# Optimization experiments

Hardware: AMD Instinct MI355X
Metric: run time of the kernel (lower is better)

## Reference

```python
import jax, jax.numpy as jnp
import numpy as np

D_MODEL = 2048
NUM_HEADS = 16
D_FF = 8192
EPS = 1e-5


def setup_inputs() -> dict:
    key = jax.random.key(0)
    ks = jax.random.split(key, 9)
    s = 0.02
    return {
        "x": jax.random.normal(ks[0], (2, 2048, D_MODEL), dtype=jnp.float32),
        "wq": jax.random.normal(ks[1], (D_MODEL, D_MODEL), dtype=jnp.float32) * s,
        "wk": jax.random.normal(ks[2], (D_MODEL, D_MODEL), dtype=jnp.float32) * s,
        "wv": jax.random.normal(ks[3], (D_MODEL, D_MODEL), dtype=jnp.float32) * s,
        "wo": jax.random.normal(ks[4], (D_MODEL, D_MODEL), dtype=jnp.float32) * s,
        "w1": jax.random.normal(ks[5], (D_FF, D_MODEL), dtype=jnp.float32) * s,
        "w2": jax.random.normal(ks[6], (D_MODEL, D_FF), dtype=jnp.float32) * s,
        "g1": jnp.ones((D_MODEL,), dtype=jnp.float32),
        "g2": jnp.ones((D_MODEL,), dtype=jnp.float32),
    }


def rmsnorm(a, g):
    rms = jnp.sqrt(jnp.sum(a * a, axis=-1, keepdims=True) / a.shape[-1] + EPS)
    return a / rms * g


def attention(xn, wq, wk, wv, wo):
    B, S, D = xn.shape
    H, dk = NUM_HEADS, D // NUM_HEADS
    # Linear weights are (out, in); y = x @ W^T
    q = (xn @ wq.T).reshape(B, S, H, dk).transpose(0, 2, 1, 3)  # bhsd
    k = (xn @ wk.T).reshape(B, S, H, dk).transpose(0, 2, 1, 3)
    v = (xn @ wv.T).reshape(B, S, H, dk).transpose(0, 2, 1, 3)
    scores = jnp.einsum("bhqd,bhkd->bhqk", q, k) * (dk ** -0.5)
    causal = jnp.triu(jnp.ones((S, S), dtype=bool), k=1)
    scores = jnp.where(causal, -jnp.inf, scores)
    probs = jax.nn.softmax(scores, axis=-1)
    out = jnp.einsum("bhqk,bhkd->bhqd", probs, v)
    out = out.transpose(0, 2, 1, 3).reshape(B, S, D)
    return out @ wo.T


def reference(x, wq, wk, wv, wo, w1, w2, g1, g2):
    x = x + attention(rmsnorm(x, g1), wq, wk, wv, wo)
    h = jax.nn.gelu(rmsnorm(x, g2) @ w1.T, approximate=False)
    x = x + h @ w2.T
    return x
```

## Files before the change

kernel.cpp:

```cpp
#include <hip/hip_runtime.h>
#include <hip/hip_bf16.h>
#include <math.h>

#define D_MODEL 2048
#define SEQ     2048
#define BATCH   2
#define NHEAD   16
#define DK      128
#define DFF     8192
#define MROWS   (BATCH*SEQ)

typedef short short8 __attribute__((ext_vector_type(8)));
typedef float f32x4  __attribute__((ext_vector_type(4)));

__device__ __forceinline__ short f2bf(float f) {
  union { __hip_bfloat16 b; short s; } u;
  u.b = __float2bfloat16(f);
  return u.s;
}

#define MF(a, b, c) __builtin_amdgcn_mfma_f32_16x16x32_bf16(a, b, c, 0, 0, 0)
#define BAR()   asm volatile("s_barrier" ::: "memory")
#define LGKM0() { asm volatile("s_waitcnt lgkmcnt(0)" ::: "memory"); __builtin_amdgcn_sched_barrier(0); }
#define STG(gptr, ldsbyte) { \
    unsigned _m0v = (unsigned)__builtin_amdgcn_readfirstlane((int)(ldsbyte)); \
    asm volatile("s_mov_b32 m0, %1\n\tglobal_load_lds_dwordx4 %0, off" \
                 :: "v"(gptr), "s"(_m0v) : "memory"); }

__global__ __launch_bounds__(256) void rmsnorm_k(const float* __restrict__ x,
                                                 const float* __restrict__ g,
                                                 short* __restrict__ o) {
  const int row = blockIdx.x;
  const int t = threadIdx.x;
  const float4* xr = (const float4*)(x + (size_t)row * D_MODEL);
  const float4* gr = (const float4*)g;
  float4 v0 = xr[2*t], v1 = xr[2*t+1];
  float s = v0.x*v0.x + v0.y*v0.y + v0.z*v0.z + v0.w*v0.w
          + v1.x*v1.x + v1.y*v1.y + v1.z*v1.z + v1.w*v1.w;
  #pragma unroll
  for (int off = 1; off < 64; off <<= 1) s += __shfl_xor(s, off);
  __shared__ float red[4];
  if ((t & 63) == 0) red[t >> 6] = s;
  __syncthreads();
  float tot = red[0] + red[1] + red[2] + red[3];
  float inv = rsqrtf(tot * (1.0f / D_MODEL) + 1e-5f);
  float4 g0 = gr[2*t], g1v = gr[2*t+1];
  short8 ov;
  ov[0] = f2bf(v0.x * inv * g0.x);
  ov[1] = f2bf(v0.y * inv * g0.y);
  ov[2] = f2bf(v0.z * inv * g0.z);
  ov[3] = f2bf(v0.w * inv * g0.w);
  ov[4] = f2bf(v1.x * inv * g1v.x);
  ov[5] = f2bf(v1.y * inv * g1v.y);
  ov[6] = f2bf(v1.z * inv * g1v.z);
  ov[7] = f2bf(v1.w * inv * g1v.w);
  *((short8*)(o + (size_t)row * D_MODEL) + t) = ov;
}

__global__ __launch_bounds__(256) void f2b_k(const float* __restrict__ src,
                                             short* __restrict__ dst, int n8) {
  int i = blockIdx.x * 256 + threadIdx.x;
  if (i >= n8) return;
  const float4* s4 = (const float4*)src + 2 * (size_t)i;
  float4 a = s4[0], b = s4[1];
  short8 o = { f2bf(a.x), f2bf(a.y), f2bf(a.z), f2bf(a.w),
               f2bf(b.x), f2bf(b.y), f2bf(b.z), f2bf(b.w) };
  *((short8*)dst + i) = o;
}

__global__ __launch_bounds__(256) void combine_k(const float* p0, const float* p1,
                                                 const float* r, float* o, int n4) {
  int i = blockIdx.x * 256 + threadIdx.x;
  if (i >= n4) return;
  const float4 a = ((const float4*)p0)[i];
  const float4 b = ((const float4*)p1)[i];
  const float4 c = ((const float4*)r)[i];
  float4 d;
  d.x = a.x + b.x + c.x; d.y = a.y + b.y + c.y;
  d.z = a.z + b.z + c.z; d.w = a.w + b.w + c.w;
  ((float4*)o)[i] = d;
}

template<int EPI, int SPLIT>
__global__ __launch_bounds__(512, 2) void gemm256(const short* __restrict__ A,
                                                  const short* __restrict__ Bp,
                                                  void* Cv,
                                                  const float* __restrict__ resid,
                                                  int M, int N, int K,
                                                  int lda, int ldb, int nbx) {
  __shared__ __align__(16) short As[2][2][128 * 64];
  __shared__ __align__(16) short Bs[2][2][128 * 64];
  const int nk = K >> 6;
  const int cpx = gridDim.x >> 3;
  const int lin = (blockIdx.x & 7) * cpx + (blockIdx.x >> 3);
  const int bx = lin % nbx;
  int row2 = lin / nbx, by, ks = 0;
  if (SPLIT) { ks = row2 & 1; by = row2 >> 1; } else { by = row2; }
  const int m0 = bx * 256, n0 = by * 256;
  if (SPLIT) { A += (size_t)ks * K; Bp += (size_t)ks * K; }

  const int t = threadIdx.x, w = t >> 6, lane = t & 63, lr = lane & 15, lg = lane >> 4;
  const int wm = w >> 2, wn = w & 3;
  const unsigned aByte = (unsigned)(size_t)(const __attribute__((address_space(3))) short*)&As[0][0][0];
  const unsigned bByte = (unsigned)(size_t)(const __attribute__((address_space(3))) short*)&Bs[0][0][0];
  const unsigned wOff = (unsigned)(w * 1024);

  const int r = t >> 3, c8 = t & 7;
  const int sw = (c8 ^ (r & 7)) << 3;
  const short* pA0 = A  + (size_t)(m0 + r)       * lda + sw;
  const short* pA1 = A  + (size_t)(m0 + 128 + r) * lda + sw;
  const short* pB0 = Bp + (size_t)(n0 + r)       * ldb + sw;
  const short* pB1 = Bp + (size_t)(n0 + 128 + r) * ldb + sw;
  const size_t l64A = (size_t)64 * lda, l64B = (size_t)64 * ldb;

  f32x4 acc[8][4];
  const f32x4 z4 = {0.f, 0.f, 0.f, 0.f};
  #pragma unroll
  for (int m = 0; m < 8; ++m)
    #pragma unroll
    for (int n = 0; n < 4; ++n) acc[m][n] = z4;

  STG(pA0,        aByte + wOff);                 STG(pA0 + l64A,      aByte + 8192 + wOff);
  STG(pA1,        aByte + 16384 + wOff);         STG(pA1 + l64A,      aByte + 16384 + 8192 + wOff);
  STG(pB0,        bByte + wOff);                 STG(pB0 + l64B,      bByte + 8192 + wOff);
  STG(pB1,        bByte + 16384 + wOff);         STG(pB1 + l64B,      bByte + 16384 + 8192 + wOff);
  if (nk > 1) {
    STG(pB0 + 64, bByte + 32768 + wOff);         STG(pB0 + 64 + l64B, bByte + 32768 + 8192 + wOff);
    STG(pB1 + 64, bByte + 32768 + 16384 + wOff); STG(pB1 + 64 + l64B, bByte + 32768 + 16384 + 8192 + wOff);
    STG(pA0 + 64, aByte + 32768 + wOff);         STG(pA0 + 64 + l64A, aByte + 32768 + 8192 + wOff);
    asm volatile("s_waitcnt vmcnt(6)" ::: "memory");
  } else {
    asm volatile("s_waitcnt vmcnt(0)" ::: "memory");
  }
  BAR();

  for (int T = 0; T < nk; ++T) {
    const int p = T & 1, q = p ^ 1;
    const unsigned aS = aByte + (unsigned)p * 32768u, aQ = aByte + (unsigned)q * 32768u;
    const unsigned bS = bByte + (unsigned)p * 32768u;

    if (T + 1 < nk) {
      const short* s = pA1 + (size_t)(T + 1) * 64;
      STG(s, aQ + 16384u + wOff); STG(s + l64A, aQ + 16384u + 8192u + wOff);
    }
    short8 bk0[4], bk1[4], aA[4];
    #pragma unroll
    for (int n = 0; n < 4; ++n) {
      int br = wn * 64 + n * 16 + lr;
      const short* bp = &Bs[p][br >> 7][(br & 127) * 64];
      bk0[n] = *(const short8*)&bp[(lg * 8)      ^ ((br & 7) << 3)];
      bk1[n] = *(const short8*)&bp[(32 + lg * 8) ^ ((br & 7) << 3)];
    }
    #pragma unroll
    for (int m = 0; m < 4; ++m) {
      int ar = m * 16 + lr;
      aA[m] = *(const short8*)&As[p][wm][ar * 64 + ((lg * 8) ^ ((ar & 7) << 3))];
    }
    BAR(); LGKM0();
    __builtin_amdgcn_s_setprio(1);
    #pragma unroll
    for (int m = 0; m < 4; ++m)
      #pragma unroll
      for (int n = 0; n < 4; ++n) acc[m][n] = MF(aA[m], bk0[n], acc[m][n]);
    __builtin_amdgcn_s_setprio(0);
    BAR();

    if (T + 2 < nk) {
      const short* s = pB0 + (size_t)(T + 2) * 64;
      STG(s, bS + wOff); STG(s + l64B, bS + 8192u + wOff);
    }
    short8 aB[4], aC[4];
    #pragma unroll
    for (int m = 0; m < 4; ++m) {
      int ar = 64 + m * 16 + lr;
      aB[m] = *(const short8*)&As[p][wm][ar * 64 + ((lg * 8) ^ ((ar & 7) << 3))];
      int ar2 = m * 16 + lr;
      aC[m] = *(const short8*)&As[p][wm][ar2 * 64 + ((32 + lg * 8) ^ ((ar2 & 7) << 3))];
    }
    BAR(); LGKM0();
    __builtin_amdgcn_s_setprio(1);
    #pragma unroll
    for (int m = 0; m < 4; ++m)
      #pragma unroll
      for (int n = 0; n < 4; ++n) acc[m + 4][n] = MF(aB[m], bk0[n], acc[m + 4][n]);
    __builtin_amdgcn_s_setprio(0);
    BAR();

    if (T + 2 < nk) {
      const short* s = pB1 + (size_t)(T + 2) * 64;
      STG(s, bS + 16384u + wOff); STG(s + l64B, bS + 16384u + 8192u + wOff);
    }
    short8 aD[4];
    #pragma unroll
    for (int m = 0; m < 4; ++m) {
      int ar = 64 + m * 16 + lr;
      aD[m] = *(const short8*)&As[p][wm][ar * 64 + ((32 + lg * 8) ^ ((ar & 7) << 3))];
    }
    BAR(); LGKM0();
    __builtin_amdgcn_s_setprio(1);
    #pragma unroll
    for (int m = 0; m < 4; ++m)
      #pragma unroll
      for (int n = 0; n < 4; ++n) acc[m][n] = MF(aC[m], bk1[n], acc[m][n]);
    __builtin_amdgcn_s_setprio(0);
    BAR();

    if (T + 2 < nk) {
      const short* s = pA0 + (size_t)(T + 2) * 64;
      STG(s, aS + wOff); STG(s + l64A, aS + 8192u + wOff);
    }
    BAR(); LGKM0();
    __builtin_amdgcn_s_setprio(1);
    #pragma unroll
    for (int m = 0; m < 4; ++m)
      #pragma unroll
      for (int n = 0; n < 4; ++n) acc[m + 4][n] = MF(aD[m], bk1[n], acc[m + 4][n]);
    __builtin_amdgcn_s_setprio(0);

    if (T + 2 < nk)      { asm volatile("s_waitcnt vmcnt(6)" ::: "memory"); BAR(); }
    else if (T + 1 < nk) { asm volatile("s_waitcnt vmcnt(0)" ::: "memory"); BAR(); }
  }

  float* Cf = (float*)Cv;
  if (SPLIT) Cf += (size_t)ks * ((size_t)M * N);
  #pragma unroll
  for (int m = 0; m < 8; ++m)
    #pragma unroll
    for (int n = 0; n < 4; ++n)
      #pragma unroll
      for (int rr = 0; rr < 4; ++rr) {
        int row = m0 + wm * 128 + m * 16 + lg * 4 + rr;
        int col = n0 + wn * 64 + n * 16 + lr;
        size_t idx = (size_t)row * N + col;
        float vv = acc[m][n][rr];
        if (EPI == 0) {
          ((short*)Cv)[idx] = f2bf(vv);
        } else if (EPI == 1) {
          float gl = 0.5f * vv * (1.0f + erff(vv * 0.70710678118654752f));
          ((short*)Cv)[idx] = f2bf(gl);
        } else if (EPI == 2) {
          ((float*)Cv)[idx] = vv + resid[idx];
        } else {
          Cf[idx] = vv;
        }
      }
}

__global__ __launch_bounds__(256) void vtrans(const short* __restrict__ QKV,
                                              short* __restrict__ VT) {
  const int st = blockIdx.x;
  const int bh = blockIdx.y;
  const int b = bh >> 4, h = bh & 15;
  const int t = threadIdx.x;
  __shared__ __align__(16) short T[64 * 128];
  const short* Vsrc = QKV + ((size_t)b * SEQ) * 6144 + 2 * D_MODEL + h * DK;
  {
    int r = t >> 4, c = (t & 15) * 8;
    #pragma unroll
    for (int i = 0; i < 4; ++i) {
      int rr = r + 16 * i;
      uint4 vv = *(const uint4*)(Vsrc + (size_t)(st * 64 + rr) * 6144 + c);
      *(uint4*)&T[rr * 128 + (c ^ (((rr >> 3) & 7) << 3))] = vv;
    }
  }
  __syncthreads();
  short* dst = VT + ((size_t)bh * DK) * SEQ + st * 64;
  {
    int c2 = (t & 7) * 8;
    #pragma unroll
    for (int i = 0; i < 4; ++i) {
      int d = (t >> 3) + 32 * i;
      short8 ov;
      #pragma unroll
      for (int j = 0; j < 8; ++j)
        ov[j] = T[(c2 + j) * 128 + (d ^ ((((c2 + j) >> 3) & 7) << 3))];
      *(short8*)(dst + (size_t)d * SEQ + c2) = ov;
    }
  }
}

__global__ __launch_bounds__(512, 2) void attn3(const short* __restrict__ QKV,
                                                const short* __restrict__ VT,
                                                short* __restrict__ O) {
  const float SC = 0.12751743f;
  const int a = blockIdx.x, bh = blockIdx.y;
  const int b = bh >> 4, h = bh & 15;
  const int t = threadIdx.x, w = t >> 6, lane = t & 63, lr = lane & 15, lg = lane >> 4;
  const short* Qp = QKV + ((size_t)b * SEQ) * 6144 + h * DK;
  const short* Kp = Qp + D_MODEL;
  const short* Vp = VT + ((size_t)bh * DK) * SEQ;
  __shared__ __align__(16) short Ks[2][64 * 128];
  __shared__ __align__(16) short Vs[2][128 * 64];
  __shared__ __align__(16) short Ps[8][16][72];

  const int krr = t >> 4, kcc = (t & 15) * 8;
  const int vdd = t >> 3, vcc = (t & 7) * 8;
  const f32x4 z4 = {0.f, 0.f, 0.f, 0.f};

  for (int sub = 0; sub < 2; ++sub) {
    const int ts = sub ? (15 - a) : a;
    const int nt = 2 * ts + 2;
    const int qrow0 = ts * 128 + w * 16;

    short8 qf[4];
    #pragma unroll
    for (int ki = 0; ki < 4; ++ki)
      qf[ki] = *(const short8*)(Qp + (size_t)(qrow0 + lr) * 6144 + ki * 32 + lg * 8);

    f32x4 acc[8];
    #pragma unroll
    for (int nd = 0; nd < 8; ++nd) acc[nd] = z4;
    float mrow[4], lsum[4];
    #pragma unroll
    for (int r = 0; r < 4; ++r) { mrow[r] = -INFINITY; lsum[r] = 0.f; }

    uint4 krg[2], vrg[2];
    #pragma unroll
    for (int i = 0; i < 2; ++i) {
      krg[i] = *(const uint4*)(Kp + (size_t)(krr + 32 * i) * 6144 + kcc);
      vrg[i] = *(const uint4*)(Vp + (size_t)(vdd + 64 * i) * SEQ + vcc);
    }
    __syncthreads();
    #pragma unroll
    for (int i = 0; i < 2; ++i) {
      int r = krr + 32 * i;
      *(uint4*)&Ks[0][(r * 128 + kcc) ^ ((r & 7) << 3)] = krg[i];
      int d = vdd + 64 * i;
      *(uint4*)&Vs[0][(d * 64 + vcc) ^ ((d & 7) << 3)] = vrg[i];
    }
    __syncthreads();

    int cur = 0;
    for (int tt = 0; tt < nt; ++tt) {
      const bool pre = (tt + 1 < nt);
      if (pre) {
        #pragma unroll
        for (int i = 0; i < 2; ++i) {
          krg[i] = *(const uint4*)(Kp + (size_t)((tt + 1) * 64 + krr + 32 * i) * 6144 + kcc);
          vrg[i] = *(const uint4*)(Vp + (size_t)(vdd + 64 * i) * SEQ + (tt + 1) * 64 + vcc);
        }
      }

      f32x4 sf[4] = {z4, z4, z4, z4};
      #pragma unroll
      for (int ki = 0; ki < 4; ++ki) {
        #pragma unroll
        for (int nk = 0; nk < 4; ++nk) {
          int rr = nk * 16 + lr;
          short8 kf = *(const short8*)&Ks[cur][(rr * 128 + ki * 32 + lg * 8) ^ ((rr & 7) << 3)];
          sf[nk] = MF(qf[ki], kf, sf[nk]);
        }
      }

      const bool diag = (tt * 64 + 63 > qrow0);
      #pragma unroll
      for (int r = 0; r < 4; ++r) {
        int qg = qrow0 + lg * 4 + r;
        float s0 = sf[0][r] * SC, s1 = sf[1][r] * SC, s2 = sf[2][r] * SC, s3 = sf[3][r] * SC;
        if (diag) {
          int c0 = tt * 64 + lr;
          s0 = (c0      <= qg) ? s0 : -3.0e38f;
          s1 = (c0 + 16 <= qg) ? s1 : -3.0e38f;
          s2 = (c0 + 32 <= qg) ? s2 : -3.0e38f;
          s3 = (c0 + 48 <= qg) ? s3 : -3.0e38f;
        }
        float mx = fmaxf(fmaxf(s0, s1), fmaxf(s2, s3));
        mx = fmaxf(mx, __shfl_xor(mx, 1));
        mx = fmaxf(mx, __shfl_xor(mx, 2));
        mx = fmaxf(mx, __shfl_xor(mx, 4));
        mx = fmaxf(mx, __shfl_xor(mx, 8));
        float mnew = fmaxf(mrow[r], mx);
        float alpha = exp2f(mrow[r] - mnew);
        mrow[r] = mnew;
        float p0 = exp2f(s0 - mnew), p1 = exp2f(s1 - mnew),
              p2 = exp2f(s2 - mnew), p3 = exp2f(s3 - mnew);
        lsum[r] = lsum[r] * alpha + ((p0 + p1) + (p2 + p3));
        #pragma unroll
        for (int nd = 0; nd < 8; ++nd) acc[nd][r] *= alpha;
        short* pr = &Ps[w][lg * 4 + r][0];
        pr[lr]      = f2bf(p0);
        pr[16 + lr] = f2bf(p1);
        pr[32 + lr] = f2bf(p2);
        pr[48 + lr] = f2bf(p3);
      }
      asm volatile("s_waitcnt lgkmcnt(0)" ::: "memory");
      __builtin_amdgcn_sched_barrier(0);

      short8 pf0 = *(const short8*)&Ps[w][lr][lg * 8];
      short8 pf1 = *(const short8*)&Ps[w][lr][32 + lg * 8];
      #pragma unroll
      for (int nd = 0; nd < 8; ++nd) {
        int rr = nd * 16 + lr;
        short8 vf0 = *(const short8*)&Vs[cur][(rr * 64 + lg * 8) ^ ((rr & 7) << 3)];
        short8 vf1 = *(const short8*)&Vs[cur][(rr * 64 + 32 + lg * 8) ^ ((rr & 7) << 3)];
        acc[nd] = MF(pf0, vf0, acc[nd]);
        acc[nd] = MF(pf1, vf1, acc[nd]);
      }
      __syncthreads();
      if (pre) {
        #pragma unroll
        for (int i = 0; i < 2; ++i) {
          int r = krr + 32 * i;
          *(uint4*)&Ks[cur ^ 1][(r * 128 + kcc) ^ ((r & 7) << 3)] = krg[i];
          int d = vdd + 64 * i;
          *(uint4*)&Vs[cur ^ 1][(d * 64 + vcc) ^ ((d & 7) << 3)] = vrg[i];
        }
      }
      __syncthreads();
      cur ^= 1;
    }

    float inv[4];
    #pragma unroll
    for (int r = 0; r < 4; ++r) {
      float ls = lsum[r];
      ls += __shfl_xor(ls, 1);
      ls += __shfl_xor(ls, 2);
      ls += __shfl_xor(ls, 4);
      ls += __shfl_xor(ls, 8);
      inv[r] = 1.0f / ls;
    }
    #pragma unroll
    for (int nd = 0; nd < 8; ++nd)
      #pragma unroll
      for (int r = 0; r < 4; ++r) {
        int row = qrow0 + lg * 4 + r;
        O[(size_t)(b * SEQ + row) * D_MODEL + h * DK + nd * 16 + lr] = f2bf(acc[nd][r] * inv[r]);
      }
  }
}

template<int EPI>
__global__ __launch_bounds__(256) void gemm_bt(const short* __restrict__ A,
                                               const float* __restrict__ B,
                                               void* Cv,
                                               const float* resid,
                                               int M, int N, int K) {
  __shared__ __align__(16) short As[128][72];
  __shared__ __align__(16) short Bs[128][72];
  const int t = threadIdx.x;
  const int m0 = blockIdx.x * 128, n0 = blockIdx.y * 128;
  const int wave = t >> 6, lane = t & 63, lr = lane & 15, lg = lane >> 4;
  const int wr = (wave >> 1) * 64, wc = (wave & 1) * 64;

  f32x4 acc[4][4];
  const f32x4 z4 = {0.f, 0.f, 0.f, 0.f};
  #pragma unroll
  for (int m = 0; m < 4; ++m)
    #pragma unroll
    for (int n = 0; n < 4; ++n) acc[m][n] = z4;

  int ar[4], ac[4];
  #pragma unroll
  for (int i = 0; i < 4; ++i) { int u = t + 256*i; ar[i] = u >> 3; ac[i] = (u & 7) * 8; }

  for (int k0 = 0; k0 < K; k0 += 64) {
    #pragma unroll
    for (int i = 0; i < 4; ++i) {
      uint4 va = *(const uint4*)(A + (size_t)(m0 + ar[i]) * K + k0 + ac[i]);
      *(uint4*)&As[ar[i]][ac[i]] = va;
    }
    #pragma unroll
    for (int i = 0; i < 4; ++i) {
      const float4* bp = (const float4*)(B + (size_t)(n0 + ar[i]) * K + k0 + ac[i]);
      float4 b0 = bp[0], b1 = bp[1];
      short8 pb = { f2bf(b0.x), f2bf(b0.y), f2bf(b0.z), f2bf(b0.w),
                    f2bf(b1.x), f2bf(b1.y), f2bf(b1.z), f2bf(b1.w) };
      *(short8*)&Bs[ar[i]][ac[i]] = pb;
    }
    __syncthreads();
    #pragma unroll
    for (int kk = 0; kk < 64; kk += 32) {
      short8 af[4], bfr[4];
      #pragma unroll
      for (int m = 0; m < 4; ++m) af[m]  = *(const short8*)&As[wr + m*16 + lr][kk + lg*8];
      #pragma unroll
      for (int n = 0; n < 4; ++n) bfr[n] = *(const short8*)&Bs[wc + n*16 + lr][kk + lg*8];
      #pragma unroll
      for (int m = 0; m < 4; ++m)
        #pragma unroll
        for (int n = 0; n < 4; ++n)
          acc[m][n] = MF(af[m], bfr[n], acc[m][n]);
    }
    __syncthreads();
  }

  #pragma unroll
  for (int m = 0; m < 4; ++m)
    #pragma unroll
    for (int n = 0; n < 4; ++n)
      #pragma unroll
      for (int r = 0; r < 4; ++r) {
        int row = m0 + wr + m*16 + lg*4 + r;
        int col = n0 + wc + n*16 + lr;
        size_t idx = (size_t)row * N + col;
        float vv = acc[m][n][r];
        if (EPI == 0) {
          ((short*)Cv)[idx] = f2bf(vv);
        } else if (EPI == 1) {
          float gl = 0.5f * vv * (1.0f + erff(vv * 0.70710678118654752f));
          ((short*)Cv)[idx] = f2bf(gl);
        } else {
          ((float*)Cv)[idx] = vv + resid[idx];
        }
      }
}

__global__ __launch_bounds__(256) void attn_k(const short* __restrict__ Q,
                                              const short* __restrict__ K,
                                              const short* __restrict__ V,
                                              short* __restrict__ O) {
  const float scale = 0.08838834764831845f;
  const int qt = blockIdx.x;
  const int bh = blockIdx.y;
  const int b = bh >> 4, h = bh & 15;
  const size_t base = ((size_t)b * SEQ) * D_MODEL + (size_t)h * DK;
  const int t = threadIdx.x, wave = t >> 6, lane = t & 63, lr = lane & 15, lg = lane >> 4;

  __shared__ __align__(16) short Ks[32][136];
  __shared__ __align__(16) short Vt[128][40];
  __shared__ __align__(16) short Ps[4][32][40];

  const int qrow0 = qt * 128 + wave * 32;
  short8 qf[2][4];
  #pragma unroll
  for (int mq = 0; mq < 2; ++mq)
    #pragma unroll
    for (int ki = 0; ki < 4; ++ki)
      qf[mq][ki] = *(const short8*)(Q + base + (size_t)(qrow0 + mq*16 + lr) * D_MODEL + ki*32 + lg*8);

  f32x4 acc[2][8];
  const f32x4 z4 = {0.f, 0.f, 0.f, 0.f};
  #pragma unroll
  for (int mq = 0; mq < 2; ++mq)
    #pragma unroll
    for (int nd = 0; nd < 8; ++nd) acc[mq][nd] = z4;
  float mrow[2][4], lsum[2][4];
  #pragma unroll
  for (int mq = 0; mq < 2; ++mq)
    #pragma unroll
    for (int r = 0; r < 4; ++r) { mrow[mq][r] = -INFINITY; lsum[mq][r] = 0.f; }

  const int lastt = qt * 4 + 3;
  for (int tt = 0; tt <= lastt; ++tt) {
    #pragma unroll
    for (int i = 0; i < 2; ++i) {
      int u = t + 256*i; int r = u >> 4; int c = (u & 15) * 8;
      *(uint4*)&Ks[r][c] = *(const uint4*)(K + base + (size_t)(tt*32 + r) * D_MODEL + c);
      uint4 vv = *(const uint4*)(V + base + (size_t)(tt*32 + r) * D_MODEL + c);
      const short* sv = (const short*)&vv;
      #pragma unroll
      for (int j = 0; j < 8; ++j) Vt[c + j][r] = sv[j];
    }
    __syncthreads();
    if (tt <= qt * 4 + wave) {
      f32x4 sf[2][2] = {{z4, z4}, {z4, z4}};
      #pragma unroll
      for (int ki = 0; ki < 4; ++ki) {
        short8 kf0 = *(const short8*)&Ks[lr][ki*32 + lg*8];
        short8 kf1 = *(const short8*)&Ks[16 + lr][ki*32 + lg*8];
        sf[0][0] = MF(qf[0][ki], kf0, sf[0][0]);
        sf[0][1] = MF(qf[0][ki], kf1, sf[0][1]);
        sf[1][0] = MF(qf[1][ki], kf0, sf[1][0]);
        sf[1][1] = MF(qf[1][ki], kf1, sf[1][1]);
      }
      #pragma unroll
      for (int mq = 0; mq < 2; ++mq) {
        #pragma unroll
        for (int r = 0; r < 4; ++r) {
          int qg = qrow0 + mq*16 + lg*4 + r;
          float s0 = sf[mq][0][r] * scale;
          float s1 = sf[mq][1][r] * scale;
          if (tt*32 + lr > qg)       s0 = -INFINITY;
          if (tt*32 + 16 + lr > qg)  s1 = -INFINITY;
          float mx = fmaxf(s0, s1);
          mx = fmaxf(mx, __shfl_xor(mx, 1));
          mx = fmaxf(mx, __shfl_xor(mx, 2));
          mx = fmaxf(mx, __shfl_xor(mx, 4));
          mx = fmaxf(mx, __shfl_xor(mx, 8));
          float mnew = fmaxf(mrow[mq][r], mx);
          float alpha = __expf(mrow[mq][r] - mnew);
          mrow[mq][r] = mnew;
          float p0 = __expf(s0 - mnew);
          float p1 = __expf(s1 - mnew);
          float ps = p0 + p1;
          ps += __shfl_xor(ps, 1);
          ps += __shfl_xor(ps, 2);
          ps += __shfl_xor(ps, 4);
          ps += __shfl_xor(ps, 8);
          lsum[mq][r] = lsum[mq][r] * alpha + ps;
          #pragma unroll
          for (int nd = 0; nd < 8; ++nd) acc[mq][nd][r] *= alpha;
          Ps[wave][mq*16 + lg*4 + r][lr]      = f2bf(p0);
          Ps[wave][mq*16 + lg*4 + r][16 + lr] = f2bf(p1);
        }
      }
      asm volatile("s_waitcnt lgkmcnt(0)" ::: "memory");
      short8 pf0 = *(const short8*)&Ps[wave][lr][lg*8];
      short8 pf1 = *(const short8*)&Ps[wave][16 + lr][lg*8];
      #pragma unroll
      for (int nd = 0; nd < 8; ++nd) {
        short8 vf = *(const short8*)&Vt[nd*16 + lr][lg*8];
        acc[0][nd] = MF(pf0, vf, acc[0][nd]);
        acc[1][nd] = MF(pf1, vf, acc[1][nd]);
      }
    }
    __syncthreads();
  }

  #pragma unroll
  for (int mq = 0; mq < 2; ++mq)
    #pragma unroll
    for (int nd = 0; nd < 8; ++nd)
      #pragma unroll
      for (int r = 0; r < 4; ++r) {
        int row = qrow0 + mq*16 + lg*4 + r;
        O[base + (size_t)row * D_MODEL + nd*16 + lr] = f2bf(acc[mq][nd][r] / lsum[mq][r]);
      }
}

extern "C" void kernel_launch(void* const* d_in, const int* in_sizes, int n_in,
                              void* d_out, int out_size, void* d_ws, size_t ws_size,
                              hipStream_t stream) {
  const float* x  = (const float*)d_in[0];
  const float* wq = (const float*)d_in[1];
  const float* wk = (const float*)d_in[2];
  const float* wv = (const float*)d_in[3];
  const float* wo = (const float*)d_in[4];
  const float* w1 = (const float*)d_in[5];
  const float* w2 = (const float*)d_in[6];
  const float* g1 = (const float*)d_in[7];
  const float* g2 = (const float*)d_in[8];
  float* out = (float*)d_out;
  char* ws = (char*)d_ws;

  const size_t NEED = (size_t)192 << 20;
  if (ws_size >= NEED) {
    short* wqkv = (short*)(ws);
    short* wo_b = (short*)(ws + ((size_t)24 << 20));
    short* w1_b = (short*)(ws + ((size_t)32 << 20));
    short* w2_b = (short*)(ws + ((size_t)64 << 20));
    short* qkv  = (short*)(ws + ((size_t)96 << 20));
    short* vt   = (short*)(ws + ((size_t)144 << 20));
    short* ab   = (short*)(ws + ((size_t)160 << 20));
    short* xn   = (short*)(ws + ((size_t)176 << 20));
    short* hb   = (short*)(ws + ((size_t)96 << 20));
    float* pf   = (float*)(ws + ((size_t)160 << 20));

    const int NW = D_MODEL * D_MODEL / 8;
    f2b_k<<<(NW + 255) / 256, 256, 0, stream>>>(wq, wqkv,                   NW);
    f2b_k<<<(NW + 255) / 256, 256, 0, stream>>>(wk, wqkv + (size_t)D_MODEL * D_MODEL,     NW);
    f2b_k<<<(NW + 255) / 256, 256, 0, stream>>>(wv, wqkv + (size_t)2 * D_MODEL * D_MODEL, NW);
    f2b_k<<<(NW + 255) / 256, 256, 0, stream>>>(wo, wo_b, NW);
    const int NF = DFF * D_MODEL / 8;
    f2b_k<<<(NF + 255) / 256, 256, 0, stream>>>(w1, w1_b, NF);
    f2b_k<<<(NF + 255) / 256, 256, 0, stream>>>(w2, w2_b, NF);

    rmsnorm_k<<<MROWS, 256, 0, stream>>>(x, g1, xn);
    gemm256<0,0><<<dim3(16 * 24), 512, 0, stream>>>(xn, wqkv, qkv, nullptr,
                                                    MROWS, 6144, D_MODEL, D_MODEL, D_MODEL, 16);
    vtrans<<<dim3(SEQ/64, BATCH*NHEAD), 256, 0, stream>>>(qkv, vt);
    attn3<<<dim3(8, BATCH*NHEAD), 512, 0, stream>>>(qkv, vt, ab);
    gemm256<2,0><<<dim3(16 * 8), 512, 0, stream>>>(ab, wo_b, out, x,
                                                   MROWS, D_MODEL, D_MODEL, D_MODEL, D_MODEL, 16);
    rmsnorm_k<<<MROWS, 256, 0, stream>>>(out, g2, xn);
    gemm256<1,0><<<dim3(16 * 32), 512, 0, stream>>>(xn, w1_b, hb, nullptr,
                                                    MROWS, DFF, D_MODEL, D_MODEL, D_MODEL, 16);
    gemm256<3,1><<<dim3(16 * 8 * 2), 512, 0, stream>>>(hb, w2_b, pf, nullptr,
                                                       MROWS, D_MODEL, DFF / 2, DFF, DFF, 16);
    const int N4 = MROWS * D_MODEL / 4;
    combine_k<<<(N4 + 255) / 256, 256, 0, stream>>>(pf, pf + (size_t)MROWS * D_MODEL, out, out, N4);
  } else {
    short* qb = (short*)(ws + ((size_t)0  << 20));
    short* kb = (short*)(ws + ((size_t)16 << 20));
    short* vb = (short*)(ws + ((size_t)32 << 20));
    short* ab = (short*)(ws + ((size_t)48 << 20));
    short* xn = (short*)(ws + ((size_t)64 << 20));
    short* hb = (short*)(ws + ((size_t)0  << 20));

    dim3 gproj(MROWS / 128, D_MODEL / 128);
    rmsnorm_k<<<MROWS, 256, 0, stream>>>(x, g1, xn);
    gemm_bt<0><<<gproj, 256, 0, stream>>>(xn, wq, qb, nullptr, MROWS, D_MODEL, D_MODEL);
    gemm_bt<0><<<gproj, 256, 0, stream>>>(xn, wk, kb, nullptr, MROWS, D_MODEL, D_MODEL);
    gemm_bt<0><<<gproj, 256, 0, stream>>>(xn, wv, vb, nullptr, MROWS, D_MODEL, D_MODEL);
    attn_k<<<dim3(SEQ / 128, BATCH * NHEAD), 256, 0, stream>>>(qb, kb, vb, ab);
    gemm_bt<2><<<gproj, 256, 0, stream>>>(ab, wo, out, x, MROWS, D_MODEL, D_MODEL);
    rmsnorm_k<<<MROWS, 256, 0, stream>>>(out, g2, xn);
    for (int half = 0; half < 2; ++half) {
      const short* xh = xn  + (size_t)half * 2048 * D_MODEL;
      float*       oh = out + (size_t)half * 2048 * D_MODEL;
      gemm_bt<1><<<dim3(2048 / 128, DFF / 128), 256, 0, stream>>>(xh, w1, hb, nullptr, 2048, DFF, D_MODEL);
      gemm_bt<2><<<dim3(2048 / 128, D_MODEL / 128), 256, 0, stream>>>(hb, w2, oh, oh, 2048, D_MODEL, DFF);
    }
  }
}
```

Before: 757.8 us.

## Replace phased ping-pong GEMM schedule with simple whole-tile double buffering

The GEMM main loop drops its four-phase schedule, which interleaved partial next-tile loads with barriers and s_setprio around each MFMA block. It now issues the entire next K-tile into the alternate LDS buffer at the start of each iteration, runs all four MFMA groups without intermediate barriers, then waits vmcnt(0) and takes one barrier. This removes several barriers per iteration and the priority toggling. In exchange it loses the prefetch depth of two tiles and the fine-grained overlap, and it forces a full memory drain every iteration.

```diff
diff --git a/kernel.cpp b/kernel.cpp
--- a/kernel.cpp
+++ b/kernel.cpp
@@ -20,8 +20,6 @@
 }
 
 #define MF(a, b, c) __builtin_amdgcn_mfma_f32_16x16x32_bf16(a, b, c, 0, 0, 0)
-#define BAR()   asm volatile("s_barrier" ::: "memory")
-#define LGKM0() { asm volatile("s_waitcnt lgkmcnt(0)" ::: "memory"); __builtin_amdgcn_sched_barrier(0); }
 #define STG(gptr, ldsbyte) { \
     unsigned _m0v = (unsigned)__builtin_amdgcn_readfirstlane((int)(ldsbyte)); \
     asm volatile("s_mov_b32 m0, %1\n\tglobal_load_lds_dwordx4 %0, off" \
@@ -113,6 +111,16 @@
   const short* pB1 = Bp + (size_t)(n0 + 128 + r) * ldb + sw;
   const size_t l64A = (size_t)64 * lda, l64B = (size_t)64 * ldb;
 
+#define STAGE_TILE(tt, slotByteA, slotByteB) { \
+    const short* a0_ = pA0 + (size_t)(tt) * 64; \
+    STG(a0_, (slotByteA) + wOff);            STG(a0_ + l64A, (slotByteA) + 8192u + wOff); \
+    const short* a1_ = pA1 + (size_t)(tt) * 64; \
+    STG(a1_, (slotByteA) + 16384u + wOff);   STG(a1_ + l64A, (slotByteA) + 16384u + 8192u + wOff); \
+    const short* b0_ = pB0 + (size_t)(tt) * 64; \
+    STG(b0_, (slotByteB) + wOff);            STG(b0_ + l64B, (slotByteB) + 8192u + wOff); \
+    const short* b1_ = pB1 + (size_t)(tt) * 64; \
+    STG(b1_, (slotByteB) + 16384u + wOff);   STG(b1_ + l64B, (slotByteB) + 16384u + 8192u + wOff); }
+
   f32x4 acc[8][4];
   const f32x4 z4 = {0.f, 0.f, 0.f, 0.f};
   #pragma unroll
@@ -120,106 +128,78 @@
     #pragma unroll
     for (int n = 0; n < 4; ++n) acc[m][n] = z4;
 
-  STG(pA0,        aByte + wOff);                 STG(pA0 + l64A,      aByte + 8192 + wOff);
-  STG(pA1,        aByte + 16384 + wOff);         STG(pA1 + l64A,      aByte + 16384 + 8192 + wOff);
-  STG(pB0,        bByte + wOff);                 STG(pB0 + l64B,      bByte + 8192 + wOff);
-  STG(pB1,        bByte + 16384 + wOff);         STG(pB1 + l64B,      bByte + 16384 + 8192 + wOff);
-  if (nk > 1) {
-    STG(pB0 + 64, bByte + 32768 + wOff);         STG(pB0 + 64 + l64B, bByte + 32768 + 8192 + wOff);
-    STG(pB1 + 64, bByte + 32768 + 16384 + wOff); STG(pB1 + 64 + l64B, bByte + 32768 + 16384 + 8192 + wOff);
-    STG(pA0 + 64, aByte + 32768 + wOff);         STG(pA0 + 64 + l64A, aByte + 32768 + 8192 + wOff);
-    asm volatile("s_waitcnt vmcnt(6)" ::: "memory");
-  } else {
-    asm volatile("s_waitcnt vmcnt(0)" ::: "memory");
-  }
-  BAR();
+  STAGE_TILE(0, aByte, bByte);
+  asm volatile("s_waitcnt vmcnt(0)" ::: "memory");
+  __builtin_amdgcn_s_barrier();
 
   for (int T = 0; T < nk; ++T) {
     const int p = T & 1, q = p ^ 1;
-    const unsigned aS = aByte + (unsigned)p * 32768u, aQ = aByte + (unsigned)q * 32768u;
-    const unsigned bS = bByte + (unsigned)p * 32768u;
-
-    if (T + 1 < nk) {
-      const short* s = pA1 + (size_t)(T + 1) * 64;
-      STG(s, aQ + 16384u + wOff); STG(s + l64A, aQ + 16384u + 8192u + wOff);
-    }
+
+    if (T + 1 < nk)
+      STAGE_TILE(T + 1, aByte + (unsigned)q * 32768u, bByte + (unsigned)q * 32768u);
+
     short8 bk0[4], bk1[4], aA[4];
     #pragma unroll
     for (int n = 0; n < 4; ++n) {
       int br = wn * 64 + n * 16 + lr;
       const short* bp = &Bs[p][br >> 7][(br & 127) * 64];
-      bk0[n] = *(const short8*)&bp[(lg * 8)      ^ ((br & 7) << 3)];
-      bk1[n] = *(const short8*)&bp[(32 + lg * 8) ^ ((br & 7) << 3)];
+      bk0[n] = *(const short8*)&bp[(lg * 8) ^ ((br & 7) << 3)];
     }
     #pragma unroll
     for (int m = 0; m < 4; ++m) {
       int ar = m * 16 + lr;
       aA[m] = *(const short8*)&As[p][wm][ar * 64 + ((lg * 8) ^ ((ar & 7) << 3))];
     }
-    BAR(); LGKM0();
-    __builtin_amdgcn_s_setprio(1);
     #pragma unroll
     for (int m = 0; m < 4; ++m)
       #pragma unroll
       for (int n = 0; n < 4; ++n) acc[m][n] = MF(aA[m], bk0[n], acc[m][n]);
-    __builtin_amdgcn_s_setprio(0);
-    BAR();
-
-    if (T + 2 < nk) {
-      const short* s = pB0 + (size_t)(T + 2) * 64;
-      STG(s, bS + wOff); STG(s + l64B, bS + 8192u + wOff);
-    }
-    short8 aB[4], aC[4];
+
+    short8 aB[4];
     #pragma unroll
     for (int m = 0; m < 4; ++m) {
       int ar = 64 + m * 16 + lr;
       aB[m] = *(const short8*)&As[p][wm][ar * 64 + ((lg * 8) ^ ((ar & 7) << 3))];
-      int ar2 = m * 16 + lr;
-      aC[m] = *(const short8*)&As[p][wm][ar2 * 64 + ((32 + lg * 8) ^ ((ar2 & 7) << 3))];
-    }
-    BAR(); LGKM0();
-    __builtin_amdgcn_s_setprio(1);
+    }
     #pragma unroll
     for (int m = 0; m < 4; ++m)
       #pragma unroll
       for (int n = 0; n < 4; ++n) acc[m + 4][n] = MF(aB[m], bk0[n], acc[m + 4][n]);
-    __builtin_amdgcn_s_setprio(0);
-    BAR();
-
-    if (T + 2 < nk) {
-      const short* s = pB1 + (size_t)(T + 2) * 64;
-      STG(s, bS + 16384u + wOff); STG(s + l64B, bS + 16384u + 8192u + wOff);
-    }
+
+    short8 aC[4];
+    #pragma unroll
+    for (int n = 0; n < 4; ++n) {
+      int br = wn * 64 + n * 16 + lr;
+      const short* bp = &Bs[p][br >> 7][(br & 127) * 64];
+      bk1[n] = *(const short8*)&bp[(32 + lg * 8) ^ ((br & 7) << 3)];
+    }
+    #pragma unroll
+    for (int m = 0; m < 4; ++m) {
+      int ar = m * 16 + lr;
+      aC[m] = *(const short8*)&As[p][wm][ar * 64 + ((32 + lg * 8) ^ ((ar & 7) << 3))];
+    }
+    #pragma unroll
+    for (int m = 0; m < 4; ++m)
+      #pragma unroll
+      for (int n = 0; n < 4; ++n) acc[m][n] = MF(aC[m], bk1[n], acc[m][n]);
+
     short8 aD[4];
     #pragma unroll
     for (int m = 0; m < 4; ++m) {
       int ar = 64 + m * 16 + lr;
       aD[m] = *(const short8*)&As[p][wm][ar * 64 + ((32 + lg * 8) ^ ((ar & 7) << 3))];
     }
-    BAR(); LGKM0();
-    __builtin_amdgcn_s_setprio(1);
     #pragma unroll
     for (int m = 0; m < 4; ++m)
       #pragma unroll
-      for (int n = 0; n < 4; ++n) acc[m][n] = MF(aC[m], bk1[n], acc[m][n]);
-    __builtin_amdgcn_s_setprio(0);
-    BAR();
-
-    if (T + 2 < nk) {
-      const short* s = pA0 + (size_t)(T + 2) * 64;
-      STG(s, aS + wOff); STG(s + l64A, aS + 8192u + wOff);
-    }
-    BAR(); LGKM0();
-    __builtin_amdgcn_s_setprio(1);
-    #pragma unroll
-    for (int m = 0; m < 4; ++m)
-      #pragma unroll
       for (int n = 0; n < 4; ++n) acc[m + 4][n] = MF(aD[m], bk1[n], acc[m + 4][n]);
-    __builtin_amdgcn_s_setprio(0);
-
-    if (T + 2 < nk)      { asm volatile("s_waitcnt vmcnt(6)" ::: "memory"); BAR(); }
-    else if (T + 1 < nk) { asm volatile("s_waitcnt vmcnt(0)" ::: "memory"); BAR(); }
+
+    if (T + 1 < nk) {
+      asm volatile("s_waitcnt vmcnt(0)" ::: "memory");
+      __builtin_amdgcn_s_barrier();
+    }
   }
+#undef STAGE_TILE
 
   float* Cf = (float*)Cv;
   if (SPLIT) Cf += (size_t)ks * ((size_t)M * N);
```

Measured after the change: 743.1 us. Within noise of the previous version (-1.9%).
